# Performance work log

Hardware: AMD Instinct MI355X
Metric: run time of the kernel (lower is better)

Reference implementation:

```python
import jax, jax.numpy as jnp
import numpy as np

T, B, H, E, V = 256, 64, 1024, 512, 32000
UNK, IGN = 2, 0
EPS = 1e-10


def setup_inputs() -> dict:
    key = jax.random.key(0)
    ks = jax.random.split(key, 16)
    s = 0.02
    return {
        'u_enc_out': jax.random.normal(ks[0], (T, B, H), jnp.float32),
        'last_hidden': jax.random.normal(ks[1], (1, B, H), jnp.float32),
        'z_tm1': jax.random.randint(ks[2], (1, B), 0, V),
        'u_input_np': jax.random.randint(ks[3], (T, B), 0, V),
        'emb_table': jax.random.normal(ks[4], (V, E), jnp.float32) * s,
        'emb_ctrl_w': jax.random.normal(ks[5], (E, E), jnp.float32) * s,
        'emb_ctrl_b': jnp.zeros((E,), jnp.float32),
        'attn_w': jax.random.normal(ks[6], (H, 2 * H), jnp.float32) * s,
        'attn_b': jnp.zeros((H,), jnp.float32),
        'attn_v': jax.random.normal(ks[7], (H,), jnp.float32) * (1.0 / np.sqrt(H)),
        'ffnn_hidden_w': jax.random.normal(ks[8], (H, 2 * H + E), jnp.float32) * s,
        'ffnn_hidden_b': jnp.zeros((H,), jnp.float32),
        'ffnn_out_w': jax.random.normal(ks[9], (V, H), jnp.float32) * s,
        'ffnn_out_b': jnp.zeros((V,), jnp.float32),
        'copy1_w': jax.random.normal(ks[10], (H, H), jnp.float32) * s,
        'copy1_b': jnp.zeros((H,), jnp.float32),
    }


def reference(u_enc_out, last_hidden, z_tm1, u_input_np, emb_table,
              emb_ctrl_w, emb_ctrl_b, attn_w, attn_b, attn_v,
              ffnn_hidden_w, ffnn_hidden_b, ffnn_out_w, ffnn_out_b,
              copy1_w, copy1_b):
    Tl, Bl, Hl = u_enc_out.shape
    Vl = ffnn_out_w.shape[0]
    enc = jnp.transpose(u_enc_out, (1, 0, 2))              # [B,T,H]
    hid = last_hidden[0]                                   # [B,H]

    # Bahdanau-style attention (Attn module)
    h_rep = jnp.broadcast_to(hid[:, None, :], enc.shape)   # [B,T,H]
    energy = jnp.tanh(jnp.concatenate([h_rep, enc], -1) @ attn_w.T + attn_b)
    att = jnp.einsum('bth,h->bt', energy, attn_v)          # [B,T]
    alpha = jax.nn.softmax(att, axis=1)
    context = jnp.einsum('bt,bth->bh', alpha, enc)         # [B,H]

    # embedding + control gate (dropout_rate=0 -> identity)
    ez = emb_table[z_tm1[0]]                               # [B,E]
    ez = (ez @ emb_ctrl_w.T + emb_ctrl_b) + ez

    ffnn_in = jnp.concatenate([ez, context, hid], -1)      # [B,E+2H]
    lh = ffnn_in @ ffnn_hidden_w.T + ffnn_hidden_b         # [B,H]
    gen_score = lh @ ffnn_out_w.T + ffnn_out_b             # [B,V]

    # copy scores over user input tokens
    ucs = jnp.tanh(enc @ copy1_w.T + copy1_b)              # [B,T,H]
    s = jnp.einsum('bth,bh->bt', ucs, lh)                  # [B,T]
    smax = jnp.max(s, axis=1, keepdims=True)
    e = jnp.exp(s - smax)                                  # [B,T]
    total = jnp.sum(e, axis=1, keepdims=True)              # [B,1]

    # scatter-aggregate exp scores by vocab id (replaces one-hot bmm)
    w = u_input_np.T                                       # [B,T]
    t_idx = jnp.arange(Tl)[None, :]
    cols = jnp.where(w == UNK, Vl + t_idx, w)
    cols = jnp.where(w == IGN, Vl + Tl, cols)              # dummy col for ignored
    agg = jnp.zeros((Bl, Vl + Tl + 1), e.dtype)
    agg = agg.at[jnp.arange(Bl)[:, None], cols].add((1.0 - EPS) * e)
    u_copy = jnp.log(EPS * total + agg[:, :Vl + Tl]) + smax  # [B,V+T]

    scores = jax.nn.softmax(jnp.concatenate([gen_score, u_copy], 1), axis=1)
    g, c = scores[:, :Vl], scores[:, Vl:]
    proba = jnp.concatenate([g + c[:, :Vl], c[:, Vl:]], 1)  # [B,V+T]
    return lh[None], proba
```

## Files before the change

kernel.cpp:

```cpp
#include <hip/hip_runtime.h>
#include <cstdint>

typedef unsigned short u16;
typedef float  f32x4  __attribute__((ext_vector_type(4)));
typedef __bf16 bf16x8 __attribute__((ext_vector_type(8)));

static constexpr int Tn = 256, Bn = 64, Hn = 1024, En = 512, Vn = 32000;
static constexpr int Mn = Tn * Bn;
static constexpr int VT = Vn + Tn;
static constexpr float EPSc = 1e-10f;

#define DEVFN __device__ __forceinline__

DEVFN u16 f2bf(float f) {
  uint32_t u = __float_as_uint(f);
  u += 0x7fffu + ((u >> 16) & 1u);
  return (u16)(u >> 16);
}
DEVFN float bf2f(u16 h) { return __uint_as_float(((uint32_t)h) << 16); }

DEVFN float tanh_fast(float x) {
  float xc = fminf(fmaxf(x, -15.f), 15.f);
  float e2 = __expf(2.f * xc);
  return __fdividef(e2 - 1.f, e2 + 1.f);
}

DEVFN float wave_rmax(float v) {
  #pragma unroll
  for (int m = 1; m < 64; m <<= 1) v = fmaxf(v, __shfl_xor(v, m));
  return v;
}
DEVFN float wave_rsum(float v) {
  #pragma unroll
  for (int m = 1; m < 64; m <<= 1) v += __shfl_xor(v, m);
  return v;
}
DEVFN float blk_rmax(float v, float* sm) {
  v = wave_rmax(v);
  if ((threadIdx.x & 63) == 0) sm[threadIdx.x >> 6] = v;
  __syncthreads();
  v = fmaxf(fmaxf(sm[0], sm[1]), fmaxf(sm[2], sm[3]));
  __syncthreads();
  return v;
}
DEVFN float blk_rsum(float v, float* sm) {
  v = wave_rsum(v);
  if ((threadIdx.x & 63) == 0) sm[threadIdx.x >> 6] = v;
  __syncthreads();
  v = sm[0] + sm[1] + sm[2] + sm[3];
  __syncthreads();
  return v;
}

__global__ __launch_bounds__(256) void k_conv_enc(const float* __restrict__ src,
                                                  u16* __restrict__ hi, u16* __restrict__ lo) {
  const int n8 = Mn * Hn / 8;
  for (int i = blockIdx.x * 256 + threadIdx.x; i < n8; i += gridDim.x * 256) {
    const float4* s4 = (const float4*)(src + (size_t)i * 8);
    float4 x0 = s4[0], x1 = s4[1];
    float xs[8] = {x0.x, x0.y, x0.z, x0.w, x1.x, x1.y, x1.z, x1.w};
    uint32_t hp[4], lp[4];
    #pragma unroll
    for (int j = 0; j < 4; ++j) {
      u16 h0 = f2bf(xs[2*j]),   h1 = f2bf(xs[2*j+1]);
      u16 l0 = f2bf(xs[2*j]   - bf2f(h0));
      u16 l1 = f2bf(xs[2*j+1] - bf2f(h1));
      hp[j] = (uint32_t)h0 | ((uint32_t)h1 << 16);
      lp[j] = (uint32_t)l0 | ((uint32_t)l1 << 16);
    }
    *(uint4*)(hi + (size_t)i * 8) = make_uint4(hp[0], hp[1], hp[2], hp[3]);
    *(uint4*)(lo + (size_t)i * 8) = make_uint4(lp[0], lp[1], lp[2], lp[3]);
  }
}

__global__ __launch_bounds__(256) void k_conv_w(const float* __restrict__ attn_w,
                                                const float* __restrict__ copy_w,
                                                u16* __restrict__ wattn,
                                                u16* __restrict__ chi, u16* __restrict__ clo) {
  const int nA = Hn * Hn / 8;
  for (int i = blockIdx.x * 256 + threadIdx.x; i < 2 * nA; i += gridDim.x * 256) {
    if (i < nA) {
      int e = i * 8; int h = e >> 10; int k = e & 1023;
      const float4* s4 = (const float4*)(attn_w + (size_t)h * 2048 + 1024 + k);
      float4 x0 = s4[0], x1 = s4[1];
      float xs[8] = {x0.x, x0.y, x0.z, x0.w, x1.x, x1.y, x1.z, x1.w};
      uint32_t hp[4];
      #pragma unroll
      for (int j = 0; j < 4; ++j)
        hp[j] = (uint32_t)f2bf(xs[2*j]) | ((uint32_t)f2bf(xs[2*j+1]) << 16);
      *(uint4*)(wattn + (size_t)i * 8) = make_uint4(hp[0], hp[1], hp[2], hp[3]);
    } else {
      int j8 = i - nA;
      const float4* s4 = (const float4*)(copy_w + (size_t)j8 * 8);
      float4 x0 = s4[0], x1 = s4[1];
      float xs[8] = {x0.x, x0.y, x0.z, x0.w, x1.x, x1.y, x1.z, x1.w};
      uint32_t hp[4], lp[4];
      #pragma unroll
      for (int j = 0; j < 4; ++j) {
        u16 h0 = f2bf(xs[2*j]),   h1 = f2bf(xs[2*j+1]);
        u16 l0 = f2bf(xs[2*j]   - bf2f(h0));
        u16 l1 = f2bf(xs[2*j+1] - bf2f(h1));
        hp[j] = (uint32_t)h0 | ((uint32_t)h1 << 16);
        lp[j] = (uint32_t)l0 | ((uint32_t)l1 << 16);
      }
      *(uint4*)(chi + (size_t)j8 * 8) = make_uint4(hp[0], hp[1], hp[2], hp[3]);
      *(uint4*)(clo + (size_t)j8 * 8) = make_uint4(lp[0], lp[1], lp[2], lp[3]);
    }
  }
}

__global__ __launch_bounds__(256) void k_init(const float* __restrict__ attn_b,
                                              const float* __restrict__ last_h,
                                              const int* __restrict__ z,
                                              const float* __restrict__ emb_t,
                                              const float* __restrict__ ectrl_b,
                                              const float* __restrict__ fh_b,
                                              float* __restrict__ hid_proj,
                                              float* __restrict__ ffnn_in,
                                              float* __restrict__ ez_emb,
                                              float* __restrict__ att,
                                              float* __restrict__ sbuf,
                                              float* __restrict__ lh_out,
                                              float* __restrict__ proba) {
  const int total = 65536 + 65536 + 32768 + 32768 + 32768 + 65536 + Bn * VT;
  for (int i = blockIdx.x * 256 + threadIdx.x; i < total; i += gridDim.x * 256) {
    int x = i;
    if (x < 65536) { hid_proj[x] = attn_b[x & 1023]; continue; }
    x -= 65536;
    if (x < 65536) { int b = x >> 10, h = x & 1023; ffnn_in[b*2560 + 1536 + h] = last_h[x]; continue; }
    x -= 65536;
    if (x < 32768) { int b = x >> 9, e = x & 511;
                     ffnn_in[b*2560 + e] = ectrl_b[e] + emb_t[(size_t)z[b]*512 + e]; continue; }
    x -= 32768;
    if (x < 32768) { int b = x >> 9, e = x & 511; ez_emb[x] = emb_t[(size_t)z[b]*512 + e]; continue; }
    x -= 32768;
    if (x < 32768) { if (x < 16384) att[x] = 0.f; else sbuf[x - 16384] = 0.f; continue; }
    x -= 32768;
    if (x < 65536) { lh_out[x] = fh_b[x & 1023]; continue; }
    x -= 65536;
    proba[x] = 0.f;
  }
}

template<bool SPLIT, bool EB, bool VB>
__global__ __launch_bounds__(256) void k_redgemm(const u16* __restrict__ Ahi, const u16* __restrict__ Alo,
                                                 const u16* __restrict__ Whi, const u16* __restrict__ Wlo,
                                                 const float* __restrict__ extra,
                                                 const float* __restrict__ vec,
                                                 float* __restrict__ out) {
  constexpr int AB = 64 * 128;
  constexpr int WB = 128 * 128;
  __shared__ uint4 ldsbuf[(SPLIT ? (2*AB + 2*WB) : (AB + WB)) / 16];
  char* ldsA  = (char*)ldsbuf;
  char* ldsAl = ldsA + AB;
  char* ldsW  = ldsA + (SPLIT ? 2*AB : AB);
  char* ldsWl = ldsW + WB;

  const int tid  = threadIdx.x;
  const int lane = tid & 63;
  const int wid  = tid >> 6;
  const int wm = wid >> 1, wn = wid & 1;
  const int lr = lane >> 4, lc = lane & 15;
  const int row0 = blockIdx.x * 64;
  const int h0   = blockIdx.y * 128;

  f32x4 z4 = {0.f, 0.f, 0.f, 0.f};
  f32x4 acc[2][4];
  #pragma unroll
  for (int i = 0; i < 2; ++i)
    #pragma unroll
    for (int j = 0; j < 4; ++j) acc[i][j] = z4;

  for (int ks = 0; ks < 16; ++ks) {
    const int k0 = ks * 64;
    #pragma unroll
    for (int i = 0; i < 2; ++i) {
      int u = tid + i * 256;
      int row = u >> 3, ch = u & 7;
      int sw = ch ^ (row & 7);
      size_t go = (size_t)(row0 + row) * 1024 + k0 + ch * 8;
      *(uint4*)(ldsA + row * 128 + sw * 16) = *(const uint4*)(Ahi + go);
      if (SPLIT) *(uint4*)(ldsAl + row * 128 + sw * 16) = *(const uint4*)(Alo + go);
    }
    #pragma unroll
    for (int i = 0; i < 4; ++i) {
      int u = tid + i * 256;
      int row = u >> 3, ch = u & 7;
      int sw = ch ^ (row & 7);
      size_t go = (size_t)(h0 + row) * 1024 + k0 + ch * 8;
      *(uint4*)(ldsW + row * 128 + sw * 16) = *(const uint4*)(Whi + go);
      if (SPLIT) *(uint4*)(ldsWl + row * 128 + sw * 16) = *(const uint4*)(Wlo + go);
    }
    __syncthreads();
    #pragma unroll
    for (int kk = 0; kk < 2; ++kk) {
      const int cg = kk * 4 + lr;
      bf16x8 ah[2], al[2], bh[4], bl[4];
      #pragma unroll
      for (int mf = 0; mf < 2; ++mf) {
        int ar = wm * 32 + mf * 16 + lc;
        int off = ar * 128 + ((cg ^ (ar & 7)) << 4);
        ah[mf] = *(const bf16x8*)(ldsA + off);
        if (SPLIT) al[mf] = *(const bf16x8*)(ldsAl + off);
      }
      #pragma unroll
      for (int nf = 0; nf < 4; ++nf) {
        int wr = wn * 64 + nf * 16 + lc;
        int off = wr * 128 + ((cg ^ (wr & 7)) << 4);
        bh[nf] = *(const bf16x8*)(ldsW + off);
        if (SPLIT) bl[nf] = *(const bf16x8*)(ldsWl + off);
      }
      #pragma unroll
      for (int mf = 0; mf < 2; ++mf)
        #pragma unroll
        for (int nf = 0; nf < 4; ++nf) {
          acc[mf][nf] = __builtin_amdgcn_mfma_f32_16x16x32_bf16(ah[mf], bh[nf], acc[mf][nf], 0, 0, 0);
          if (SPLIT) {
            acc[mf][nf] = __builtin_amdgcn_mfma_f32_16x16x32_bf16(al[mf], bh[nf], acc[mf][nf], 0, 0, 0);
            acc[mf][nf] = __builtin_amdgcn_mfma_f32_16x16x32_bf16(ah[mf], bl[nf], acc[mf][nf], 0, 0, 0);
          }
        }
    }
    __syncthreads();
  }

  #pragma unroll
  for (int mf = 0; mf < 2; ++mf) {
    #pragma unroll
    for (int r = 0; r < 4; ++r) {
      int ml = wm * 32 + mf * 16 + lr * 4 + r;
      float sum = 0.f;
      #pragma unroll
      for (int nf = 0; nf < 4; ++nf) {
        int h = h0 + wn * 64 + nf * 16 + lc;
        float x = acc[mf][nf][r] + (EB ? extra[ml * 1024 + h] : extra[h]);
        sum += tanh_fast(x) * (VB ? vec[ml * 1024 + h] : vec[h]);
      }
      #pragma unroll
      for (int mM = 1; mM < 16; mM <<= 1) sum += __shfl_xor(sum, mM);
      if (lc == 0) atomicAdd(&out[row0 + ml], sum);
    }
  }
}

template<bool ATOMIC, bool BIAS>
__global__ __launch_bounds__(256) void k_sgemm(const float* __restrict__ A, int lda,
                                               const float* __restrict__ W, int ldw,
                                               float* __restrict__ out, int ldo,
                                               const float* __restrict__ bias, int kchunk) {
  __shared__ float Asm[32][68];
  __shared__ float Wsm[32][132];
  const int tid = threadIdx.x;
  const int bg = tid >> 5, ng = tid & 31;
  const int n0 = blockIdx.x * 128;
  const int kbeg = blockIdx.y * kchunk;

  float acc[8][4];
  #pragma unroll
  for (int i = 0; i < 8; ++i)
    #pragma unroll
    for (int j = 0; j < 4; ++j) acc[i][j] = 0.f;

  for (int k0 = kbeg; k0 < kbeg + kchunk; k0 += 32) {
    #pragma unroll
    for (int i = 0; i < 8; ++i) {
      int u = tid + i * 256; int b = u >> 5, kk = u & 31;
      Asm[kk][b] = A[(size_t)b * lda + k0 + kk];
    }
    #pragma unroll
    for (int i = 0; i < 16; ++i) {
      int u = tid + i * 256; int n = u >> 5, kk = u & 31;
      Wsm[kk][n] = W[(size_t)(n0 + n) * ldw + k0 + kk];
    }
    __syncthreads();
    #pragma unroll 4
    for (int kk = 0; kk < 32; ++kk) {
      float4 a0 = *(const float4*)&Asm[kk][bg * 8];
      float4 a1 = *(const float4*)&Asm[kk][bg * 8 + 4];
      float4 w  = *(const float4*)&Wsm[kk][ng * 4];
      float av[8] = {a0.x, a0.y, a0.z, a0.w, a1.x, a1.y, a1.z, a1.w};
      float wv[4] = {w.x, w.y, w.z, w.w};
      #pragma unroll
      for (int ii = 0; ii < 8; ++ii)
        #pragma unroll
        for (int jj = 0; jj < 4; ++jj) acc[ii][jj] = fmaf(av[ii], wv[jj], acc[ii][jj]);
    }
    __syncthreads();
  }
  #pragma unroll
  for (int ii = 0; ii < 8; ++ii) {
    int b = bg * 8 + ii;
    #pragma unroll
    for (int jj = 0; jj < 4; ++jj) {
      int n = n0 + ng * 4 + jj;
      float v = acc[ii][jj];
      if (BIAS) v += bias[n];
      if (ATOMIC) atomicAdd(&out[(size_t)b * ldo + n], v);
      else out[(size_t)b * ldo + n] = v;
    }
  }
}

__global__ __launch_bounds__(256) void k_rowsoftmax(const float* __restrict__ att, float* __restrict__ alpha) {
  __shared__ float sm[4];
  int b = blockIdx.x, t = threadIdx.x;
  float v = att[t * 64 + b];
  float mx = blk_rmax(v, sm);
  float e = __expf(v - mx);
  float s = blk_rsum(e, sm);
  alpha[b * 256 + t] = e / s;
}

__global__ __launch_bounds__(256) void k_context(const float* __restrict__ enc, const float* __restrict__ alpha,
                                                 float* __restrict__ ffnn_in) {
  __shared__ float al[256];
  int b = blockIdx.y;
  int h = blockIdx.x * 256 + threadIdx.x;
  al[threadIdx.x] = alpha[b * 256 + threadIdx.x];
  __syncthreads();
  float acc = 0.f;
  #pragma unroll 4
  for (int t = 0; t < 256; ++t)
    acc = fmaf(al[t], enc[((size_t)t * 64 + b) * 1024 + h], acc);
  ffnn_in[b * 2560 + 512 + h] = acc;
}

__global__ __launch_bounds__(256) void k_copyprep(const float* __restrict__ sbuf, const int* __restrict__ u_inp,
                                                  float* __restrict__ proba, float* __restrict__ smax_a,
                                                  float* __restrict__ total_a, float* __restrict__ sagg_a) {
  __shared__ float sm[4];
  int b = blockIdx.x, t = threadIdx.x;
  float sv = sbuf[t * 64 + b];
  float mx = blk_rmax(sv, sm);
  float e = __expf(sv - mx);
  float tot = blk_rsum(e, sm);
  int w = u_inp[t * 64 + b];
  float sni = blk_rsum((w != 0) ? e : 0.f, sm);
  if (w != 0) {
    int col = (w == 2) ? (Vn + t) : w;
    atomicAdd(&proba[(size_t)b * VT + col], (1.f - EPSc) * e);
  }
  if (t == 0) { smax_a[b] = mx; total_a[b] = tot; sagg_a[b] = (1.f - EPSc) * sni; }
}

__global__ __launch_bounds__(256) void k_finalA(const float* __restrict__ gen, const float* __restrict__ proba,
                                                const float* __restrict__ smax_a, const float* __restrict__ total_a,
                                                const float* __restrict__ sagg_a,
                                                float* __restrict__ m_a, float* __restrict__ fac_a,
                                                float* __restrict__ invD_a) {
  __shared__ float sm[4];
  int b = blockIdx.x, t = threadIdx.x;
  float gm = -3.4e38f;
  for (int j = t; j < Vn; j += 256) gm = fmaxf(gm, gen[(size_t)b * Vn + j]);
  gm = blk_rmax(gm, sm);
  float am = 0.f;
  for (int j = t; j < VT; j += 256) am = fmaxf(am, proba[(size_t)b * VT + j]);
  am = blk_rmax(am, sm);
  float smax = smax_a[b], tot = total_a[b];
  float m = fmaxf(gm, smax + logf(EPSc * tot + am));
  float se = 0.f;
  for (int j = t; j < Vn; j += 256) se += __expf(gen[(size_t)b * Vn + j] - m);
  se = blk_rsum(se, sm);
  if (t == 0) {
    float fac = __expf(smax - m);
    float D = se + fac * (EPSc * tot * (float)VT + sagg_a[b]);
    m_a[b] = m; fac_a[b] = fac; invD_a[b] = 1.f / D;
  }
}

__global__ __launch_bounds__(256) void k_finalB(const float* __restrict__ gen,
                                                const float* __restrict__ m_a, const float* __restrict__ fac_a,
                                                const float* __restrict__ invD_a, const float* __restrict__ total_a,
                                                float* __restrict__ proba) {
  int b = blockIdx.y;
  int j = blockIdx.x * 256 + threadIdx.x;
  size_t idx = (size_t)b * VT + j;
  float agg = proba[idx];
  float p = (EPSc * total_a[b] + agg) * fac_a[b];
  if (j < Vn) p += __expf(gen[(size_t)b * Vn + j] - m_a[b]);
  proba[idx] = p * invD_a[b];
}

extern "C" void kernel_launch(void* const* d_in, const int* in_sizes, int n_in,
                              void* d_out, int out_size, void* d_ws, size_t ws_size,
                              hipStream_t stream) {
  (void)in_sizes; (void)n_in; (void)out_size; (void)ws_size;
  const float* u_enc   = (const float*)d_in[0];
  const float* last_h  = (const float*)d_in[1];
  const int*   z_tm1   = (const int*)d_in[2];
  const int*   u_inp   = (const int*)d_in[3];
  const float* emb_t   = (const float*)d_in[4];
  const float* ectrl_w = (const float*)d_in[5];
  const float* ectrl_b = (const float*)d_in[6];
  const float* attn_w  = (const float*)d_in[7];
  const float* attn_b  = (const float*)d_in[8];
  const float* attn_v  = (const float*)d_in[9];
  const float* fh_w    = (const float*)d_in[10];
  const float* fh_b    = (const float*)d_in[11];
  const float* fo_w    = (const float*)d_in[12];
  const float* fo_b    = (const float*)d_in[13];
  const float* c1_w    = (const float*)d_in[14];
  const float* c1_b    = (const float*)d_in[15];

  float* lh_out = (float*)d_out;
  float* proba  = (float*)d_out + 65536;

  char* ws = (char*)d_ws;
  u16*  enc_hi   = (u16*)(ws + 0);
  u16*  enc_lo   = (u16*)(ws + 33554432);
  u16*  w_attn   = (u16*)(ws + 67108864);
  u16*  w_chi    = (u16*)(ws + 69206016);
  u16*  w_clo    = (u16*)(ws + 71303168);
  float* hid_proj= (float*)(ws + 73400320);
  float* ffnn_in = (float*)(ws + 73662464);
  float* ez_emb  = (float*)(ws + 74317824);
  float* att     = (float*)(ws + 74448896);
  float* sbuf    = (float*)(ws + 74514432);
  float* alpha   = (float*)(ws + 74579968);
  float* gen     = (float*)(ws + 74645504);
  float* smax_a  = (float*)(ws + 82837504);
  float* total_a = smax_a + 64;
  float* sagg_a  = smax_a + 128;
  float* m_a     = smax_a + 192;
  float* fac_a   = smax_a + 256;
  float* invD_a  = smax_a + 320;

  k_conv_enc<<<2048, 256, 0, stream>>>(u_enc, enc_hi, enc_lo);
  k_conv_w<<<1024, 256, 0, stream>>>(attn_w, c1_w, w_attn, w_chi, w_clo);
  k_init<<<4096, 256, 0, stream>>>(attn_b, last_h, z_tm1, emb_t, ectrl_b, fh_b,
                                   hid_proj, ffnn_in, ez_emb, att, sbuf, lh_out, proba);
  k_sgemm<true,  false><<<dim3(8, 8),   256, 0, stream>>>(last_h, 1024, attn_w, 2048, hid_proj, 1024, nullptr, 128);
  k_redgemm<false, true, false><<<dim3(256, 8), 256, 0, stream>>>(enc_hi, nullptr, w_attn, nullptr,
                                                                  hid_proj, attn_v, att);
  k_rowsoftmax<<<64, 256, 0, stream>>>(att, alpha);
  k_context<<<dim3(4, 64), 256, 0, stream>>>(u_enc, alpha, ffnn_in);
  k_sgemm<true,  false><<<dim3(4, 4),   256, 0, stream>>>(ez_emb, 512, ectrl_w, 512, ffnn_in, 2560, nullptr, 128);
  k_sgemm<true,  false><<<dim3(8, 8),   256, 0, stream>>>(ffnn_in, 2560, fh_w, 2560, lh_out, 1024, nullptr, 320);
  k_sgemm<false, true ><<<dim3(250, 1), 256, 0, stream>>>(lh_out, 1024, fo_w, 1024, gen, 32000, fo_b, 1024);
  k_redgemm<true, false, true><<<dim3(256, 8), 256, 0, stream>>>(enc_hi, enc_lo, w_chi, w_clo,
                                                                 c1_b, lh_out, sbuf);
  k_copyprep<<<64, 256, 0, stream>>>(sbuf, u_inp, proba, smax_a, total_a, sagg_a);
  k_finalA<<<64, 256, 0, stream>>>(gen, proba, smax_a, total_a, sagg_a, m_a, fac_a, invD_a);
  k_finalB<<<dim3(126, 64), 256, 0, stream>>>(gen, m_a, fac_a, invD_a, total_a, proba);
}
```

Before: 1.100 ms.

## Prefetch redgemm tiles, add dedicated gen GEMM, split final softmax into parallel stages

The bf16 MFMA reduction GEMM now precomputes its addresses and prefetches the next K-slab into registers while the current slab is computed, so global load latency overlaps the math. The vocab projection moves from the generic sgemm launch of 250 blocks to a dedicated 64x64-tile register-blocked kernel with 500 blocks and a register prefetch. The final softmax pass, which used 64 blocks to reduce over 32k columns, is split into partial-max, combine, partial-sum and scale kernels with 8 chunks per row, which raises parallelism at the cost of more launches and one extra pass over proba.

```diff
diff --git a/kernel.cpp b/kernel.cpp
--- a/kernel.cpp
+++ b/kernel.cpp
@@ -164,6 +164,35 @@
   const int row0 = blockIdx.x * 64;
   const int h0   = blockIdx.y * 128;
 
+  int alds[2]; size_t aoff[2];
+  #pragma unroll
+  for (int i = 0; i < 2; ++i) {
+    int u = tid + i * 256, row = u >> 3, ch = u & 7;
+    alds[i] = row * 128 + ((ch ^ (row & 7)) << 4);
+    aoff[i] = (size_t)(row0 + row) * 1024 + ch * 8;
+  }
+  int wlds[4]; size_t woff[4];
+  #pragma unroll
+  for (int i = 0; i < 4; ++i) {
+    int u = tid + i * 256, row = u >> 3, ch = u & 7;
+    wlds[i] = row * 128 + ((ch ^ (row & 7)) << 4);
+    woff[i] = (size_t)(h0 + row) * 1024 + ch * 8;
+  }
+
+  uint4 pah[2], pal[2], pwh[4], pwl[4];
+  auto loadstage = [&](int k0) {
+    #pragma unroll
+    for (int i = 0; i < 2; ++i) {
+      pah[i] = *(const uint4*)(Ahi + aoff[i] + k0);
+      if (SPLIT) pal[i] = *(const uint4*)(Alo + aoff[i] + k0);
+    }
+    #pragma unroll
+    for (int i = 0; i < 4; ++i) {
+      pwh[i] = *(const uint4*)(Whi + woff[i] + k0);
+      if (SPLIT) pwl[i] = *(const uint4*)(Wlo + woff[i] + k0);
+    }
+  };
+
   f32x4 z4 = {0.f, 0.f, 0.f, 0.f};
   f32x4 acc[2][4];
   #pragma unroll
@@ -171,27 +200,20 @@
     #pragma unroll
     for (int j = 0; j < 4; ++j) acc[i][j] = z4;
 
+  loadstage(0);
   for (int ks = 0; ks < 16; ++ks) {
-    const int k0 = ks * 64;
     #pragma unroll
     for (int i = 0; i < 2; ++i) {
-      int u = tid + i * 256;
-      int row = u >> 3, ch = u & 7;
-      int sw = ch ^ (row & 7);
-      size_t go = (size_t)(row0 + row) * 1024 + k0 + ch * 8;
-      *(uint4*)(ldsA + row * 128 + sw * 16) = *(const uint4*)(Ahi + go);
-      if (SPLIT) *(uint4*)(ldsAl + row * 128 + sw * 16) = *(const uint4*)(Alo + go);
+      *(uint4*)(ldsA + alds[i]) = pah[i];
+      if (SPLIT) *(uint4*)(ldsAl + alds[i]) = pal[i];
     }
     #pragma unroll
     for (int i = 0; i < 4; ++i) {
-      int u = tid + i * 256;
-      int row = u >> 3, ch = u & 7;
-      int sw = ch ^ (row & 7);
-      size_t go = (size_t)(h0 + row) * 1024 + k0 + ch * 8;
-      *(uint4*)(ldsW + row * 128 + sw * 16) = *(const uint4*)(Whi + go);
-      if (SPLIT) *(uint4*)(ldsWl + row * 128 + sw * 16) = *(const uint4*)(Wlo + go);
+      *(uint4*)(ldsW + wlds[i]) = pwh[i];
+      if (SPLIT) *(uint4*)(ldsWl + wlds[i]) = pwl[i];
     }
     __syncthreads();
+    if (ks < 15) loadstage((ks + 1) * 64);
     #pragma unroll
     for (int kk = 0; kk < 2; ++kk) {
       const int cg = kk * 4 + lr;
@@ -299,6 +321,72 @@
       else out[(size_t)b * ldo + n] = v;
     }
   }
+}
+
+__global__ __launch_bounds__(256) void k_gen(const float* __restrict__ lh,
+                                             const float* __restrict__ W,
+                                             const float* __restrict__ bias,
+                                             float* __restrict__ out) {
+  __shared__ float lsm[64][36];
+  __shared__ float wsm[64][36];
+  const int t = threadIdx.x;
+  const int tn = t & 15, tb = t >> 4;
+  const int n0 = blockIdx.x * 64;
+  const int r0 = t >> 3, c0 = t & 7;
+
+  const float* lp0 = lh + r0 * 1024 + c0 * 4;
+  const float* lp1 = lh + (r0 + 32) * 1024 + c0 * 4;
+  const float* wp0 = W + (size_t)(n0 + r0) * 1024 + c0 * 4;
+  const float* wp1 = W + (size_t)(n0 + r0 + 32) * 1024 + c0 * 4;
+
+  float4 pl0 = *(const float4*)lp0, pl1 = *(const float4*)lp1;
+  float4 pw0 = *(const float4*)wp0, pw1 = *(const float4*)wp1;
+
+  float acc[4][4];
+  #pragma unroll
+  for (int i = 0; i < 4; ++i)
+    #pragma unroll
+    for (int j = 0; j < 4; ++j) acc[i][j] = 0.f;
+
+  for (int k0 = 0; k0 < 1024; k0 += 32) {
+    *(float4*)&lsm[r0][c0 * 4]      = pl0;
+    *(float4*)&lsm[r0 + 32][c0 * 4] = pl1;
+    *(float4*)&wsm[r0][c0 * 4]      = pw0;
+    *(float4*)&wsm[r0 + 32][c0 * 4] = pw1;
+    __syncthreads();
+    if (k0 < 992) {
+      pl0 = *(const float4*)(lp0 + k0 + 32);
+      pl1 = *(const float4*)(lp1 + k0 + 32);
+      pw0 = *(const float4*)(wp0 + k0 + 32);
+      pw1 = *(const float4*)(wp1 + k0 + 32);
+    }
+    #pragma unroll
+    for (int kk = 0; kk < 32; kk += 4) {
+      float4 a[4], w[4];
+      #pragma unroll
+      for (int i = 0; i < 4; ++i) a[i] = *(const float4*)&lsm[tb + 16 * i][kk];
+      #pragma unroll
+      for (int j = 0; j < 4; ++j) w[j] = *(const float4*)&wsm[tn + 16 * j][kk];
+      #pragma unroll
+      for (int i = 0; i < 4; ++i)
+        #pragma unroll
+        for (int j = 0; j < 4; ++j) {
+          acc[i][j] = fmaf(a[i].x, w[j].x, acc[i][j]);
+          acc[i][j] = fmaf(a[i].y, w[j].y, acc[i][j]);
+          acc[i][j] = fmaf(a[i].z, w[j].z, acc[i][j]);
+          acc[i][j] = fmaf(a[i].w, w[j].w, acc[i][j]);
+        }
+    }
+    __syncthreads();
+  }
+  float bj[4];
+  #pragma unroll
+  for (int j = 0; j < 4; ++j) bj[j] = bias[n0 + tn + 16 * j];
+  #pragma unroll
+  for (int i = 0; i < 4; ++i)
+    #pragma unroll
+    for (int j = 0; j < 4; ++j)
+      out[(size_t)(tb + 16 * i) * 32000 + n0 + tn + 16 * j] = acc[i][j] + bj[j];
 }
 
 __global__ __launch_bounds__(256) void k_rowsoftmax(const float* __restrict__ att, float* __restrict__ alpha) {
@@ -327,7 +415,7 @@
 
 __global__ __launch_bounds__(256) void k_copyprep(const float* __restrict__ sbuf, const int* __restrict__ u_inp,
                                                   float* __restrict__ proba, float* __restrict__ smax_a,
-                                                  float* __restrict__ total_a, float* __restrict__ sagg_a) {
+                                                  float* __restrict__ total_a) {
   __shared__ float sm[4];
   int b = blockIdx.x, t = threadIdx.x;
   float sv = sbuf[t * 64 + b];
@@ -335,50 +423,64 @@
   float e = __expf(sv - mx);
   float tot = blk_rsum(e, sm);
   int w = u_inp[t * 64 + b];
-  float sni = blk_rsum((w != 0) ? e : 0.f, sm);
   if (w != 0) {
     int col = (w == 2) ? (Vn + t) : w;
     atomicAdd(&proba[(size_t)b * VT + col], (1.f - EPSc) * e);
   }
-  if (t == 0) { smax_a[b] = mx; total_a[b] = tot; sagg_a[b] = (1.f - EPSc) * sni; }
-}
-
-__global__ __launch_bounds__(256) void k_finalA(const float* __restrict__ gen, const float* __restrict__ proba,
-                                                const float* __restrict__ smax_a, const float* __restrict__ total_a,
-                                                const float* __restrict__ sagg_a,
-                                                float* __restrict__ m_a, float* __restrict__ fac_a,
-                                                float* __restrict__ invD_a) {
+  if (t == 0) { smax_a[b] = mx; total_a[b] = tot; }
+}
+
+__global__ __launch_bounds__(256) void k_fmaxp(const float* __restrict__ gen, const float* __restrict__ proba,
+                                               float* __restrict__ gm_p, float* __restrict__ am_p) {
   __shared__ float sm[4];
-  int b = blockIdx.x, t = threadIdx.x;
+  int b = blockIdx.x, c = blockIdx.y, t = threadIdx.x;
   float gm = -3.4e38f;
-  for (int j = t; j < Vn; j += 256) gm = fmaxf(gm, gen[(size_t)b * Vn + j]);
+  for (int j = c * 4000 + t; j < (c + 1) * 4000; j += 256) gm = fmaxf(gm, gen[(size_t)b * Vn + j]);
   gm = blk_rmax(gm, sm);
   float am = 0.f;
-  for (int j = t; j < VT; j += 256) am = fmaxf(am, proba[(size_t)b * VT + j]);
+  for (int j = c * 4032 + t; j < (c + 1) * 4032; j += 256) am = fmaxf(am, proba[(size_t)b * VT + j]);
   am = blk_rmax(am, sm);
-  float smax = smax_a[b], tot = total_a[b];
-  float m = fmaxf(gm, smax + logf(EPSc * tot + am));
-  float se = 0.f;
-  for (int j = t; j < Vn; j += 256) se += __expf(gen[(size_t)b * Vn + j] - m);
-  se = blk_rsum(se, sm);
-  if (t == 0) {
-    float fac = __expf(smax - m);
-    float D = se + fac * (EPSc * tot * (float)VT + sagg_a[b]);
-    m_a[b] = m; fac_a[b] = fac; invD_a[b] = 1.f / D;
-  }
-}
-
-__global__ __launch_bounds__(256) void k_finalB(const float* __restrict__ gen,
-                                                const float* __restrict__ m_a, const float* __restrict__ fac_a,
-                                                const float* __restrict__ invD_a, const float* __restrict__ total_a,
-                                                float* __restrict__ proba) {
+  if (t == 0) { gm_p[b * 8 + c] = gm; am_p[b * 8 + c] = am; }
+}
+
+__global__ __launch_bounds__(64) void k_fcomb(const float* __restrict__ gm_p, const float* __restrict__ am_p,
+                                              const float* __restrict__ smax_a, const float* __restrict__ total_a,
+                                              float* __restrict__ m_a, float* __restrict__ fac_a) {
+  int b = threadIdx.x;
+  float gm = -3.4e38f, am = 0.f;
+  #pragma unroll
+  for (int c = 0; c < 8; ++c) { gm = fmaxf(gm, gm_p[b * 8 + c]); am = fmaxf(am, am_p[b * 8 + c]); }
+  float m = fmaxf(gm, smax_a[b] + logf(EPSc * total_a[b] + am));
+  m_a[b] = m;
+  fac_a[b] = __expf(smax_a[b] - m);
+}
+
+__global__ __launch_bounds__(256) void k_fsum(const float* __restrict__ gen,
+                                              const float* __restrict__ m_a, const float* __restrict__ fac_a,
+                                              const float* __restrict__ total_a,
+                                              float* __restrict__ proba, float* __restrict__ se_p) {
+  __shared__ float sm[4];
+  int b = blockIdx.x, c = blockIdx.y, t = threadIdx.x;
+  float m = m_a[b], fac = fac_a[b], et = EPSc * total_a[b];
+  float s = 0.f;
+  for (int j = c * 4032 + t; j < (c + 1) * 4032; j += 256) {
+    size_t idx = (size_t)b * VT + j;
+    float p = (et + proba[idx]) * fac;
+    if (j < Vn) p += __expf(gen[(size_t)b * Vn + j] - m);
+    proba[idx] = p;
+    s += p;
+  }
+  s = blk_rsum(s, sm);
+  if (t == 0) se_p[b * 8 + c] = s;
+}
+
+__global__ __launch_bounds__(256) void k_fscale(const float* __restrict__ se_p, float* __restrict__ proba) {
   int b = blockIdx.y;
   int j = blockIdx.x * 256 + threadIdx.x;
-  size_t idx = (size_t)b * VT + j;
-  float agg = proba[idx];
-  float p = (EPSc * total_a[b] + agg) * fac_a[b];
-  if (j < Vn) p += __expf(gen[(size_t)b * Vn + j] - m_a[b]);
-  proba[idx] = p * invD_a[b];
+  float D = 0.f;
+  #pragma unroll
+  for (int c = 0; c < 8; ++c) D += se_p[b * 8 + c];
+  proba[(size_t)b * VT + j] *= 1.f / D;
 }
 
 extern "C" void kernel_launch(void* const* d_in, const int* in_sizes, int n_in,
@@ -420,10 +522,11 @@
   float* gen     = (float*)(ws + 74645504);
   float* smax_a  = (float*)(ws + 82837504);
   float* total_a = smax_a + 64;
-  float* sagg_a  = smax_a + 128;
-  float* m_a     = smax_a + 192;
-  float* fac_a   = smax_a + 256;
-  float* invD_a  = smax_a + 320;
+  float* m_a     = smax_a + 128;
+  float* fac_a   = smax_a + 192;
+  float* gm_p    = (float*)(ws + 74612736);
+  float* am_p    = gm_p + 512;
+  float* se_p    = gm_p + 1024;
 
   k_conv_enc<<<2048, 256, 0, stream>>>(u_enc, enc_hi, enc_lo);
   k_conv_w<<<1024, 256, 0, stream>>>(attn_w, c1_w, w_attn, w_chi, w_clo);
@@ -436,10 +539,12 @@
   k_context<<<dim3(4, 64), 256, 0, stream>>>(u_enc, alpha, ffnn_in);
   k_sgemm<true,  false><<<dim3(4, 4),   256, 0, stream>>>(ez_emb, 512, ectrl_w, 512, ffnn_in, 2560, nullptr, 128);
   k_sgemm<true,  false><<<dim3(8, 8),   256, 0, stream>>>(ffnn_in, 2560, fh_w, 2560, lh_out, 1024, nullptr, 320);
-  k_sgemm<false, true ><<<dim3(250, 1), 256, 0, stream>>>(lh_out, 1024, fo_w, 1024, gen, 32000, fo_b, 1024);
+  k_gen<<<500, 256, 0, stream>>>(lh_out, fo_w, fo_b, gen);
   k_redgemm<true, false, true><<<dim3(256, 8), 256, 0, stream>>>(enc_hi, enc_lo, w_chi, w_clo,
                                                                  c1_b, lh_out, sbuf);
-  k_copyprep<<<64, 256, 0, stream>>>(sbuf, u_inp, proba, smax_a, total_a, sagg_a);
-  k_finalA<<<64, 256, 0, stream>>>(gen, proba, smax_a, total_a, sagg_a, m_a, fac_a, invD_a);
-  k_finalB<<<dim3(126, 64), 256, 0, stream>>>(gen, m_a, fac_a, invD_a, total_a, proba);
-}
+  k_copyprep<<<64, 256, 0, stream>>>(sbuf, u_inp, proba, smax_a, total_a);
+  k_fmaxp<<<dim3(64, 8), 256, 0, stream>>>(gen, proba, gm_p, am_p);
+  k_fcomb<<<1, 64, 0, stream>>>(gm_p, am_p, smax_a, total_a, m_a, fac_a);
+  k_fsum<<<dim3(64, 8), 256, 0, stream>>>(gen, m_a, fac_a, total_a, proba, se_p);
+  k_fscale<<<dim3(126, 64), 256, 0, stream>>>(se_p, proba);
+}
```

Result: slower. 1.364 ms (+24.0%).
